# Performance work log

Hardware: AMD Instinct MI355X
Metric: run time of the kernel (lower is better)

The kernel has to match this reference:

```python
import jax, jax.numpy as jnp
import numpy as np

B, C, L = 16, 256, 2048

def setup_inputs() -> dict:
    key = jax.random.key(0)
    y = jax.random.normal(key, (B, C, L), dtype=jnp.float32)
    alpha = jnp.float32(0.5)
    beta = jnp.float32(0.5)
    gamma = jnp.float32(0.0)
    return {"y": y, "alpha": alpha, "beta": beta, "gamma": gamma}

def reference(y, alpha, beta, gamma):
    # y: [B, C, L]
    Bs, Cs, Ls = y.shape
    # channel attention: scores over channels, scaled by 1/sqrt(L)
    scale_c = 1.0 / np.sqrt(max(Ls, 1)).astype(np.float32)
    scores_c = jnp.einsum('bcl,bdl->bcd', y, y) * scale_c          # [B, C, C]
    attn_c = jax.nn.softmax(scores_c, axis=-1)
    y_c = jnp.einsum('bcd,bdl->bcl', attn_c, y)                    # [B, C, L]
    # time attention: scores over time steps, scaled by 1/sqrt(C)
    scale_t = 1.0 / np.sqrt(max(Cs, 1)).astype(np.float32)
    scores_t = jnp.einsum('bcl,bcm->blm', y, y) * scale_t          # [B, L, L]
    attn_t = jax.nn.softmax(scores_t, axis=-1)
    y_t = jnp.einsum('blm,bcm->bcl', attn_t, y)                    # [B, C, L]
    # learnable weighted combine + residual (gamma)
    out = alpha * y_c + beta * y_t + gamma * y
    return out
```

## Files before the change

kernel.cpp:

```cpp
#include <hip/hip_runtime.h>

#define B_ 16
#define C_ 256
#define L_ 2048

typedef __attribute__((ext_vector_type(8))) short short8;
typedef __attribute__((ext_vector_type(4))) float float4v;

__device__ inline float4v mfma16(short8 a, short8 b, float4v c) {
  return __builtin_amdgcn_mfma_f32_16x16x32_bf16(a, b, c, 0, 0, 0);
}

__device__ inline ushort f2bf(float x) {
  union { float f; unsigned u; } v; v.f = x;
  unsigned r = (v.u + 0x7fffu + ((v.u >> 16) & 1u)) >> 16;
  return (ushort)r;
}

__device__ inline float bf2f(ushort u) {
  union { unsigned u; float f; } v; v.u = ((unsigned)u) << 16;
  return v.f;
}

__device__ inline void dma16(const ushort* g, void* l) {
  __builtin_amdgcn_global_load_lds(
      (const __attribute__((address_space(1))) unsigned int*)(g),
      (__attribute__((address_space(3))) unsigned int*)(l), 16, 0, 0);
}

#define BAR_FULL() asm volatile("s_waitcnt vmcnt(0) lgkmcnt(0)\ns_barrier" ::: "memory")
#define BAR_LGKM() asm volatile("s_waitcnt lgkmcnt(0)\ns_barrier" ::: "memory")
#define BAR_VM8() asm volatile("s_waitcnt vmcnt(8)\ns_barrier" ::: "memory")
#define BAR_VM4() asm volatile("s_waitcnt vmcnt(4)\ns_barrier" ::: "memory")
#define BAR_VM0() asm volatile("s_waitcnt vmcnt(0)\ns_barrier" ::: "memory")
#define BAR_RAW() asm volatile("s_barrier" ::: "memory")

__global__ __launch_bounds__(256) void cvt_kernel(const float* __restrict__ y,
                                                  ushort* __restrict__ yb,
                                                  ushort* __restrict__ ytb) {
  __shared__ float tile[64][68];
  int b = blockIdx.z, ct = blockIdx.y, lt = blockIdx.x;
  int tx = threadIdx.x & 15, ty = threadIdx.x >> 4;
  size_t base = ((size_t)b * C_ + (size_t)ct * 64) * L_ + (size_t)lt * 64;
#pragma unroll
  for (int i = 0; i < 4; ++i) {
    int r = ty + i * 16;
    float4 v = *(const float4*)(y + base + (size_t)r * L_ + tx * 4);
    *(float4*)(&tile[r][tx * 4]) = v;
    ushort4 u;
    u.x = f2bf(v.x); u.y = f2bf(v.y); u.z = f2bf(v.z); u.w = f2bf(v.w);
    *(ushort4*)(yb + base + (size_t)r * L_ + tx * 4) = u;
  }
  __syncthreads();
  size_t tbase = ((size_t)b * L_ + (size_t)lt * 64) * C_ + (size_t)ct * 64;
#pragma unroll
  for (int i = 0; i < 4; ++i) {
    int r = ty + i * 16;
    ushort4 u;
    u.x = f2bf(tile[tx * 4 + 0][r]);
    u.y = f2bf(tile[tx * 4 + 1][r]);
    u.z = f2bf(tile[tx * 4 + 2][r]);
    u.w = f2bf(tile[tx * 4 + 3][r]);
    *(ushort4*)(ytb + tbase + (size_t)r * C_ + tx * 4) = u;
  }
}

__global__ __launch_bounds__(512) void pk_kernel(const ushort* __restrict__ yb,
                                                 ushort* __restrict__ Pc,
                                                 float* __restrict__ ginvC) {
  const int blk = blockIdx.x;
  const int b = (blk & 7) + 8 * ((blk >> 3) & 1);
  const int m0 = (blk >> 4) * 16;
  const int tid = threadIdx.x;
  const int w = tid >> 6, lane = tid & 63, quad = lane >> 4, l16 = lane & 15;
  const float scale = 0.022097086912079608f;
  const float SHIFT = 45.0f;

  __shared__ __align__(16) unsigned char Tb[3][32768];
  __shared__ float wsum[8][16];

  const ushort* Yb = yb + (size_t)b * C_ * L_;
  const int chq = ((lane & 3) - ((lane >> 3) & 3)) & 3;
  const int dl = (lane >> 2) * L_ + chq * 8;
  const int sK = (quad + ((l16 >> 1) & 3)) & 3;
  const int frag_lane = l16 * 64 + sK * 16;

  float4v acc[2];
#pragma unroll
  for (int nt = 0; nt < 2; ++nt) acc[nt] = (float4v){0.f, 0.f, 0.f, 0.f};

  auto PK_STAGE = [&](int t) {
    int kc = t * 64;
    unsigned char* bp = Tb[t % 3];
#pragma unroll
    for (int j = 0; j < 4; ++j) {
      int gi = w * 4 + j, kk2 = gi >> 4, chgrp = gi & 15;
      dma16(Yb + (size_t)chgrp * 16 * L_ + kc + kk2 * 32 + dl, (void*)(bp + gi * 1024));
    }
  };

  PK_STAGE(0);
  PK_STAGE(1);

  for (int c = 0; c < 32; ++c) {
    if (c == 31) { BAR_VM0(); } else { BAR_VM4(); }
    if (c < 30) PK_STAGE(c + 2);
    const unsigned char* cbuf = Tb[c % 3];
    __builtin_amdgcn_s_setprio(1);
#pragma unroll
    for (int kk2 = 0; kk2 < 2; ++kk2) {
      short8 aA = *(const short8*)(cbuf + (kk2 * 16 + (m0 >> 4)) * 1024 + frag_lane);
#pragma unroll
      for (int nt = 0; nt < 2; ++nt) {
        short8 bB = *(const short8*)(cbuf + (kk2 * 16 + w * 2 + nt) * 1024 + frag_lane);
        acc[nt] = mfma16(aA, bB, acc[nt]);
      }
    }
    __builtin_amdgcn_s_setprio(0);
  }

  float p[2][4], rs[4] = {0.f, 0.f, 0.f, 0.f};
#pragma unroll
  for (int nt = 0; nt < 2; ++nt)
#pragma unroll
    for (int r = 0; r < 4; ++r) {
      p[nt][r] = __expf(fmaf(acc[nt][r], scale, -SHIFT));
      rs[r] += p[nt][r];
    }
  ushort* Pb = Pc + ((size_t)b * 256 + m0) * 256;
#pragma unroll
  for (int nt = 0; nt < 2; ++nt)
#pragma unroll
    for (int r = 0; r < 4; ++r)
      Pb[(quad * 4 + r) * 256 + w * 32 + nt * 16 + l16] = f2bf(p[nt][r]);
#pragma unroll
  for (int r = 0; r < 4; ++r)
#pragma unroll
    for (int off = 1; off < 16; off <<= 1) rs[r] += __shfl_xor(rs[r], off);
  if (l16 == 0) {
#pragma unroll
    for (int r = 0; r < 4; ++r) wsum[w][quad * 4 + r] = rs[r];
  }
  __syncthreads();
  if (tid < 16) {
    float s = 0.f;
#pragma unroll
    for (int ww = 0; ww < 8; ++ww) s += wsum[ww][tid];
    ginvC[b * 256 + m0 + tid] = 1.0f / s;
  }
}

__global__ __launch_bounds__(256, 2) void ct_kernel(
    const ushort* __restrict__ yb, const ushort* __restrict__ ytb,
    const ushort* __restrict__ Pc, const float* __restrict__ ginvC,
    float* __restrict__ out, const float* __restrict__ alpha_p,
    const float* __restrict__ beta_p, const float* __restrict__ gamma_p) {
  const int blk = blockIdx.x;
  const int b = (blk & 7) + 8 * ((blk >> 3) & 1);
  const int m0 = (blk >> 4) * 64;
  const int tid = threadIdx.x;
  const int w = tid >> 6, lane = tid & 63, quad = lane >> 4, l16 = lane & 15;
  const int mtw = w >> 1, kt2 = w & 1;
  const float scale = 0.0625f;
  const float SHIFT = 16.0f;

  __shared__ __align__(16) unsigned char buf[2][32768];
  __shared__ ushort Pd[64 * 40];
  __shared__ float wsum[4][64];
  __shared__ float ginv[64];

  const ushort* Yt = ytb + (size_t)b * L_ * C_;
  const ushort* Yb = yb + (size_t)b * C_ * L_;
  const ushort* Pcb = Pc + (size_t)b * 256 * 256;
  const int chq = ((lane & 3) - ((lane >> 3) & 3)) & 3;
  const int klK = (lane >> 2) * C_ + chq * 8;
  const int vlV = (lane >> 2) * L_ + chq * 8;
  const int pcl = (lane >> 2) * 256 + chq * 8;
  const int sK = (quad + ((l16 >> 1) & 3)) & 3;
  const int frag_lane = l16 * 64 + sK * 16;

  short8 Qf[2][8];
#pragma unroll
  for (int mt = 0; mt < 2; ++mt)
#pragma unroll
    for (int kk = 0; kk < 8; ++kk)
      Qf[mt][kk] = *(const short8*)(Yt + (size_t)(m0 + mtw * 32 + mt * 16 + l16) * C_ +
                                    kk * 32 + quad * 8);
  const ushort* qgrow[2];
#pragma unroll
  for (int mt = 0; mt < 2; ++mt)
    qgrow[mt] = Yt + (size_t)(m0 + (1 - mtw) * 32 + mt * 16 + l16) * C_ + quad * 8;

  float4v fc[4][4];
#pragma unroll
  for (int mt = 0; mt < 4; ++mt)
#pragma unroll
    for (int nt = 0; nt < 4; ++nt) fc[mt][nt] = (float4v){0.f, 0.f, 0.f, 0.f};

  short8 qg[2][2];
#pragma unroll
  for (int mt = 0; mt < 2; ++mt) qg[0][mt] = *(const short8*)(qgrow[mt]);
#pragma unroll
  for (int j = 0; j < 4; ++j) {
    int gi = w * 4 + j;
    dma16(Pcb + (size_t)(gi * 16) * 256 + pcl, (void*)(buf[0] + gi * 1024));
  }

  for (int c2 = 0; c2 < 8; ++c2) {
    const int cb = c2 & 1;
    BAR_FULL();
    if (c2 < 7) {
      unsigned char* bp = buf[cb ^ 1];
#pragma unroll
      for (int j = 0; j < 4; ++j) {
        int gi = w * 4 + j;
        dma16(Pcb + (size_t)(gi * 16) * 256 + (c2 + 1) * 32 + pcl,
              (void*)(bp + gi * 1024));
      }
#pragma unroll
      for (int mt = 0; mt < 2; ++mt)
        qg[cb ^ 1][mt] = *(const short8*)(qgrow[mt] + (c2 + 1) * 32);
    }
    __builtin_amdgcn_s_setprio(1);
#pragma unroll
    for (int mt = 0; mt < 4; ++mt) {
      short8 Ac = *(const short8*)(buf[cb] + (w * 4 + mt) * 1024 + frag_lane);
#pragma unroll
      for (int nt = 0; nt < 4; ++nt) {
        short8 Bq = ((nt >> 1) == mtw) ? Qf[nt & 1][c2] : qg[cb][nt & 1];
        fc[mt][nt] = mfma16(Ac, Bq, fc[mt][nt]);
      }
    }
    __builtin_amdgcn_s_setprio(0);
  }

  const ushort* dp[8];
#pragma unroll
  for (int j = 0; j < 8; ++j) {
    int gi = w * 8 + j;
    if (gi < 16) {
      int kk = gi >> 1, g = gi & 1;
      dp[j] = Yt + (size_t)(g * 16) * C_ + kk * 32 + klK;
    } else {
      int cg = gi - 16;
      dp[j] = Yb + (size_t)cg * 16 * L_ + vlV;
    }
  }
  const int dstride = (w < 2) ? 32 * C_ : 32;

  float4v ft[4][4];
#pragma unroll
  for (int mt = 0; mt < 4; ++mt)
#pragma unroll
    for (int nt = 0; nt < 4; ++nt) ft[mt][nt] = (float4v){0.f, 0.f, 0.f, 0.f};
  float rs[2][4] = {{0.f, 0.f, 0.f, 0.f}, {0.f, 0.f, 0.f, 0.f}};

#pragma unroll
  for (int j = 0; j < 8; ++j) {
    dma16(dp[j], (void*)(buf[0] + (w * 8 + j) * 1024));
    dp[j] += dstride;
  }
  BAR_RAW();
#pragma unroll
  for (int j = 0; j < 8; ++j) {
    dma16(dp[j], (void*)(buf[1] + (w * 8 + j) * 1024));
    dp[j] += dstride;
  }

  for (int c = 0; c < 64; ++c) {
    const int cb = c & 1;
    if (c == 63) { BAR_VM0(); } else { BAR_VM8(); }
    float4v s0 = (float4v){0.f, 0.f, 0.f, 0.f};
    float4v s1 = (float4v){0.f, 0.f, 0.f, 0.f};
    __builtin_amdgcn_s_setprio(1);
#pragma unroll
    for (int kk = 0; kk < 8; ++kk) {
      short8 bf = *(const short8*)(buf[cb] + (kk * 2 + kt2) * 1024 + frag_lane);
      s0 = mfma16(Qf[0][kk], bf, s0);
      s1 = mfma16(Qf[1][kk], bf, s1);
    }
    __builtin_amdgcn_s_setprio(0);
#pragma unroll
    for (int mt = 0; mt < 2; ++mt) {
      float4v s = mt ? s1 : s0;
#pragma unroll
      for (int r = 0; r < 4; ++r) {
        float p = __expf(fmaf(s[r], scale, -SHIFT));
        rs[mt][r] += p;
        Pd[(mtw * 32 + mt * 16 + quad * 4 + r) * 40 + kt2 * 16 + l16] = f2bf(p);
      }
    }
    BAR_LGKM();
    __builtin_amdgcn_s_setprio(1);
#pragma unroll
    for (int mt = 0; mt < 4; ++mt) {
      short8 va = *(const short8*)(buf[cb] + (16 + w * 4 + mt) * 1024 + frag_lane);
#pragma unroll
      for (int nt = 0; nt < 4; ++nt) {
        short8 pb = *(const short8*)(&Pd[(nt * 16 + l16) * 40 + quad * 8]);
        ft[mt][nt] = mfma16(va, pb, ft[mt][nt]);
      }
    }
    __builtin_amdgcn_s_setprio(0);
    BAR_RAW();
    if (c < 62) {
#pragma unroll
      for (int j = 0; j < 8; ++j) {
        dma16(dp[j], (void*)(buf[cb] + (w * 8 + j) * 1024));
        dp[j] += dstride;
      }
    }
  }

  __syncthreads();
#pragma unroll
  for (int mt = 0; mt < 2; ++mt)
#pragma unroll
    for (int r = 0; r < 4; ++r)
#pragma unroll
      for (int off = 1; off < 16; off <<= 1) rs[mt][r] += __shfl_xor(rs[mt][r], off);
  if (l16 == 0) {
#pragma unroll
    for (int mt = 0; mt < 2; ++mt)
#pragma unroll
      for (int r = 0; r < 4; ++r)
        wsum[w][mtw * 32 + mt * 16 + quad * 4 + r] = rs[mt][r];
  }
  __syncthreads();
  if (tid < 64) {
    int mh = tid >> 5;
    ginv[tid] = 1.0f / (wsum[mh * 2][tid] + wsum[mh * 2 + 1][tid]);
  }
  __syncthreads();

  const float alpha = alpha_p[0], beta = beta_p[0], gamma = gamma_p[0];
  float gq[4];
#pragma unroll
  for (int nt = 0; nt < 4; ++nt) gq[nt] = beta * ginv[nt * 16 + l16];
  float gc[4][4];
#pragma unroll
  for (int mt = 0; mt < 4; ++mt)
#pragma unroll
    for (int r = 0; r < 4; ++r)
      gc[mt][r] = alpha * ginvC[b * 256 + w * 64 + mt * 16 + quad * 4 + r];

  if (gamma != 0.0f) {
#pragma unroll
    for (int mt = 0; mt < 4; ++mt)
#pragma unroll
      for (int nt = 0; nt < 4; ++nt)
#pragma unroll
        for (int r = 0; r < 4; ++r) {
          int ch = w * 64 + mt * 16 + quad * 4 + r;
          size_t idx = ((size_t)b * C_ + ch) * L_ + m0 + nt * 16 + l16;
          float v = gc[mt][r] * fc[mt][nt][r] + gq[nt] * ft[mt][nt][r];
          out[idx] = fmaf(gamma, bf2f(Yb[(size_t)ch * L_ + m0 + nt * 16 + l16]), v);
        }
  } else {
#pragma unroll
    for (int mt = 0; mt < 4; ++mt)
#pragma unroll
      for (int nt = 0; nt < 4; ++nt)
#pragma unroll
        for (int r = 0; r < 4; ++r) {
          int ch = w * 64 + mt * 16 + quad * 4 + r;
          size_t idx = ((size_t)b * C_ + ch) * L_ + m0 + nt * 16 + l16;
          out[idx] = gc[mt][r] * fc[mt][nt][r] + gq[nt] * ft[mt][nt][r];
        }
  }
}

extern "C" void kernel_launch(void* const* d_in, const int* in_sizes, int n_in,
                              void* d_out, int out_size, void* d_ws, size_t ws_size,
                              hipStream_t stream) {
  const float* y = (const float*)d_in[0];
  const float* alpha = (const float*)d_in[1];
  const float* beta = (const float*)d_in[2];
  const float* gamma = (const float*)d_in[3];
  float* out = (float*)d_out;

  ushort* yb = (ushort*)d_ws;
  ushort* ytb = yb + (size_t)B_ * C_ * L_;
  ushort* Pc = ytb + (size_t)B_ * C_ * L_;
  float* ginvC = (float*)(Pc + (size_t)B_ * 256 * 256);

  hipLaunchKernelGGL(cvt_kernel, dim3(L_ / 64, C_ / 64, B_), dim3(256), 0, stream,
                     y, yb, ytb);
  hipLaunchKernelGGL(pk_kernel, dim3(256), dim3(512), 0, stream, yb, Pc, ginvC);
  hipLaunchKernelGGL(ct_kernel, dim3(512), dim3(256), 0, stream,
                     yb, ytb, Pc, ginvC, out, alpha, beta, gamma);
}
```

Measured before the change: 205.1 us.

## Give each wave its own 16 query columns, passing P through registers

Restructures ct_kernel so each wave owns 16 query time steps across all 256 channels instead of a 2x2 split of queries and key halves. The softmax probabilities now go straight from the score MFMA output registers into the PV MFMA operand, with no LDS staging buffer. This removes the per-iteration LDS write/read and one barrier, and shrinks the row-sum reduction to a single LDS pass. It also reworks the Pc prefetch into a two-deep DMA pipeline and permutes K row loading to match the register layout. In exchange each wave loads all 16 K tiles and all 16 V tiles per step, so LDS read traffic per wave grows. It also relies on a register-layout trick and on lgkm-only waits in place of barriers, which must be correct.

```diff
diff --git a/kernel.cpp b/kernel.cpp
--- a/kernel.cpp
+++ b/kernel.cpp
@@ -29,11 +29,12 @@
 }
 
 #define BAR_FULL() asm volatile("s_waitcnt vmcnt(0) lgkmcnt(0)\ns_barrier" ::: "memory")
-#define BAR_LGKM() asm volatile("s_waitcnt lgkmcnt(0)\ns_barrier" ::: "memory")
 #define BAR_VM8() asm volatile("s_waitcnt vmcnt(8)\ns_barrier" ::: "memory")
 #define BAR_VM4() asm volatile("s_waitcnt vmcnt(4)\ns_barrier" ::: "memory")
 #define BAR_VM0() asm volatile("s_waitcnt vmcnt(0)\ns_barrier" ::: "memory")
 #define BAR_RAW() asm volatile("s_barrier" ::: "memory")
+#define WAIT_VM0() asm volatile("s_waitcnt vmcnt(0)" ::: "memory")
+#define WAIT_LGKM0() asm volatile("s_waitcnt lgkmcnt(0)" ::: "memory")
 
 __global__ __launch_bounds__(256) void cvt_kernel(const float* __restrict__ y,
                                                   ushort* __restrict__ yb,
@@ -160,79 +161,26 @@
   const int m0 = (blk >> 4) * 64;
   const int tid = threadIdx.x;
   const int w = tid >> 6, lane = tid & 63, quad = lane >> 4, l16 = lane & 15;
-  const int mtw = w >> 1, kt2 = w & 1;
-  const float scale = 0.0625f;
+  const float scale_t = 0.0625f;
   const float SHIFT = 16.0f;
 
   __shared__ __align__(16) unsigned char buf[2][32768];
-  __shared__ ushort Pd[64 * 40];
-  __shared__ float wsum[4][64];
-  __shared__ float ginv[64];
+  __shared__ float rsum[256];
 
   const ushort* Yt = ytb + (size_t)b * L_ * C_;
   const ushort* Yb = yb + (size_t)b * C_ * L_;
   const ushort* Pcb = Pc + (size_t)b * 256 * 256;
   const int chq = ((lane & 3) - ((lane >> 3) & 3)) & 3;
-  const int klK = (lane >> 2) * C_ + chq * 8;
   const int vlV = (lane >> 2) * L_ + chq * 8;
   const int pcl = (lane >> 2) * 256 + chq * 8;
   const int sK = (quad + ((l16 >> 1) & 3)) & 3;
   const int frag_lane = l16 * 64 + sK * 16;
-
-  short8 Qf[2][8];
-#pragma unroll
-  for (int mt = 0; mt < 2; ++mt)
-#pragma unroll
-    for (int kk = 0; kk < 8; ++kk)
-      Qf[mt][kk] = *(const short8*)(Yt + (size_t)(m0 + mtw * 32 + mt * 16 + l16) * C_ +
-                                    kk * 32 + quad * 8);
-  const ushort* qgrow[2];
-#pragma unroll
-  for (int mt = 0; mt < 2; ++mt)
-    qgrow[mt] = Yt + (size_t)(m0 + (1 - mtw) * 32 + mt * 16 + l16) * C_ + quad * 8;
-
-  float4v fc[4][4];
-#pragma unroll
-  for (int mt = 0; mt < 4; ++mt)
-#pragma unroll
-    for (int nt = 0; nt < 4; ++nt) fc[mt][nt] = (float4v){0.f, 0.f, 0.f, 0.f};
-
-  short8 qg[2][2];
-#pragma unroll
-  for (int mt = 0; mt < 2; ++mt) qg[0][mt] = *(const short8*)(qgrow[mt]);
-#pragma unroll
-  for (int j = 0; j < 4; ++j) {
-    int gi = w * 4 + j;
-    dma16(Pcb + (size_t)(gi * 16) * 256 + pcl, (void*)(buf[0] + gi * 1024));
-  }
-
-  for (int c2 = 0; c2 < 8; ++c2) {
-    const int cb = c2 & 1;
-    BAR_FULL();
-    if (c2 < 7) {
-      unsigned char* bp = buf[cb ^ 1];
-#pragma unroll
-      for (int j = 0; j < 4; ++j) {
-        int gi = w * 4 + j;
-        dma16(Pcb + (size_t)(gi * 16) * 256 + (c2 + 1) * 32 + pcl,
-              (void*)(bp + gi * 1024));
-      }
-#pragma unroll
-      for (int mt = 0; mt < 2; ++mt)
-        qg[cb ^ 1][mt] = *(const short8*)(qgrow[mt] + (c2 + 1) * 32);
-    }
-    __builtin_amdgcn_s_setprio(1);
-#pragma unroll
-    for (int mt = 0; mt < 4; ++mt) {
-      short8 Ac = *(const short8*)(buf[cb] + (w * 4 + mt) * 1024 + frag_lane);
-#pragma unroll
-      for (int nt = 0; nt < 4; ++nt) {
-        short8 Bq = ((nt >> 1) == mtw) ? Qf[nt & 1][c2] : qg[cb][nt & 1];
-        fc[mt][nt] = mfma16(Ac, Bq, fc[mt][nt]);
-      }
-    }
-    __builtin_amdgcn_s_setprio(0);
-  }
+  const int qcol = m0 + w * 16 + l16;
+
+  short8 Qf[8];
+#pragma unroll
+  for (int kk = 0; kk < 8; ++kk)
+    Qf[kk] = *(const short8*)(Yt + (size_t)qcol * C_ + kk * 32 + quad * 8);
 
   const ushort* dp[8];
 #pragma unroll
@@ -240,7 +188,9 @@
     int gi = w * 8 + j;
     if (gi < 16) {
       int kk = gi >> 1, g = gi & 1;
-      dp[j] = Yt + (size_t)(g * 16) * C_ + kk * 32 + klK;
+      int ridx = lane >> 2;
+      int trow = g * 4 + (ridx & 3) + (ridx >> 2) * 8;
+      dp[j] = Yt + (size_t)trow * C_ + kk * 32 + chq * 8;
     } else {
       int cg = gi - 16;
       dp[j] = Yb + (size_t)cg * 16 * L_ + vlV;
@@ -248,24 +198,60 @@
   }
   const int dstride = (w < 2) ? 32 * C_ : 32;
 
-  float4v ft[4][4];
-#pragma unroll
-  for (int mt = 0; mt < 4; ++mt)
-#pragma unroll
-    for (int nt = 0; nt < 4; ++nt) ft[mt][nt] = (float4v){0.f, 0.f, 0.f, 0.f};
-  float rs[2][4] = {{0.f, 0.f, 0.f, 0.f}, {0.f, 0.f, 0.f, 0.f}};
-
-#pragma unroll
-  for (int j = 0; j < 8; ++j) {
-    dma16(dp[j], (void*)(buf[0] + (w * 8 + j) * 1024));
-    dp[j] += dstride;
-  }
-  BAR_RAW();
+  WAIT_VM0();
+
+  float4v fc[16];
+#pragma unroll
+  for (int ct = 0; ct < 16; ++ct) fc[ct] = (float4v){0.f, 0.f, 0.f, 0.f};
+
+#pragma unroll
+  for (int j = 0; j < 4; ++j) {
+    int gi = w * 4 + j;
+    dma16(Pcb + (size_t)(gi * 16) * 256 + pcl, (void*)(buf[0] + gi * 1024));
+  }
+#pragma unroll
+  for (int j = 0; j < 4; ++j) {
+    int gi = w * 4 + j;
+    dma16(Pcb + (size_t)(gi * 16) * 256 + 32 + pcl, (void*)(buf[1] + gi * 1024));
+  }
+
+  for (int c2 = 0; c2 < 8; ++c2) {
+    const int cb = c2 & 1;
+    if (c2 == 7) { BAR_VM0(); } else { BAR_VM4(); }
+    if (c2 == 7) {
+#pragma unroll
+      for (int j = 0; j < 8; ++j) {
+        dma16(dp[j], (void*)(buf[0] + (w * 8 + j) * 1024));
+        dp[j] += dstride;
+      }
+    }
+    __builtin_amdgcn_s_setprio(1);
+#pragma unroll
+    for (int ct = 0; ct < 16; ++ct) {
+      short8 Ac = *(const short8*)(buf[cb] + ct * 1024 + frag_lane);
+      fc[ct] = mfma16(Ac, Qf[c2], fc[ct]);
+    }
+    __builtin_amdgcn_s_setprio(0);
+    BAR_RAW();
+    if (c2 < 6) {
+#pragma unroll
+      for (int j = 0; j < 4; ++j) {
+        int gi = w * 4 + j;
+        dma16(Pcb + (size_t)(gi * 16) * 256 + (c2 + 2) * 32 + pcl,
+              (void*)(buf[cb] + gi * 1024));
+      }
+    }
+  }
 #pragma unroll
   for (int j = 0; j < 8; ++j) {
     dma16(dp[j], (void*)(buf[1] + (w * 8 + j) * 1024));
     dp[j] += dstride;
   }
+
+  float4v ft[16];
+#pragma unroll
+  for (int ct = 0; ct < 16; ++ct) ft[ct] = (float4v){0.f, 0.f, 0.f, 0.f};
+  float rs = 0.f;
 
   for (int c = 0; c < 64; ++c) {
     const int cb = c & 1;
@@ -275,31 +261,28 @@
     __builtin_amdgcn_s_setprio(1);
 #pragma unroll
     for (int kk = 0; kk < 8; ++kk) {
-      short8 bf = *(const short8*)(buf[cb] + (kk * 2 + kt2) * 1024 + frag_lane);
-      s0 = mfma16(Qf[0][kk], bf, s0);
-      s1 = mfma16(Qf[1][kk], bf, s1);
+      short8 k0 = *(const short8*)(buf[cb] + (kk * 2 + 0) * 1024 + frag_lane);
+      short8 k1 = *(const short8*)(buf[cb] + (kk * 2 + 1) * 1024 + frag_lane);
+      s0 = mfma16(k0, Qf[kk], s0);
+      s1 = mfma16(k1, Qf[kk], s1);
     }
     __builtin_amdgcn_s_setprio(0);
-#pragma unroll
-    for (int mt = 0; mt < 2; ++mt) {
-      float4v s = mt ? s1 : s0;
-#pragma unroll
-      for (int r = 0; r < 4; ++r) {
-        float p = __expf(fmaf(s[r], scale, -SHIFT));
-        rs[mt][r] += p;
-        Pd[(mtw * 32 + mt * 16 + quad * 4 + r) * 40 + kt2 * 16 + l16] = f2bf(p);
-      }
-    }
-    BAR_LGKM();
+    union PU { ushort us[8]; short8 v; } pu;
+    float p0, p1;
+#pragma unroll
+    for (int r = 0; r < 4; ++r) {
+      p0 = __expf(fmaf(s0[r], scale_t, -SHIFT));
+      p1 = __expf(fmaf(s1[r], scale_t, -SHIFT));
+      rs += p0 + p1;
+      pu.us[r] = f2bf(p0);
+      pu.us[4 + r] = f2bf(p1);
+    }
+    short8 pb = pu.v;
     __builtin_amdgcn_s_setprio(1);
 #pragma unroll
-    for (int mt = 0; mt < 4; ++mt) {
-      short8 va = *(const short8*)(buf[cb] + (16 + w * 4 + mt) * 1024 + frag_lane);
-#pragma unroll
-      for (int nt = 0; nt < 4; ++nt) {
-        short8 pb = *(const short8*)(&Pd[(nt * 16 + l16) * 40 + quad * 8]);
-        ft[mt][nt] = mfma16(va, pb, ft[mt][nt]);
-      }
+    for (int ct = 0; ct < 16; ++ct) {
+      short8 va = *(const short8*)(buf[cb] + (16 + ct) * 1024 + frag_lane);
+      ft[ct] = mfma16(va, pb, ft[ct]);
     }
     __builtin_amdgcn_s_setprio(0);
     BAR_RAW();
@@ -312,61 +295,39 @@
     }
   }
 
-  __syncthreads();
-#pragma unroll
-  for (int mt = 0; mt < 2; ++mt)
-#pragma unroll
-    for (int r = 0; r < 4; ++r)
-#pragma unroll
-      for (int off = 1; off < 16; off <<= 1) rs[mt][r] += __shfl_xor(rs[mt][r], off);
-  if (l16 == 0) {
-#pragma unroll
-    for (int mt = 0; mt < 2; ++mt)
-#pragma unroll
-      for (int r = 0; r < 4; ++r)
-        wsum[w][mtw * 32 + mt * 16 + quad * 4 + r] = rs[mt][r];
-  }
-  __syncthreads();
-  if (tid < 64) {
-    int mh = tid >> 5;
-    ginv[tid] = 1.0f / (wsum[mh * 2][tid] + wsum[mh * 2 + 1][tid]);
-  }
-  __syncthreads();
+  rsum[tid] = rs;
+  WAIT_LGKM0();
+  float rstot = rsum[w * 64 + l16] + rsum[w * 64 + 16 + l16] +
+                rsum[w * 64 + 32 + l16] + rsum[w * 64 + 48 + l16];
 
   const float alpha = alpha_p[0], beta = beta_p[0], gamma = gamma_p[0];
-  float gq[4];
-#pragma unroll
-  for (int nt = 0; nt < 4; ++nt) gq[nt] = beta * ginv[nt * 16 + l16];
-  float gc[4][4];
-#pragma unroll
-  for (int mt = 0; mt < 4; ++mt)
-#pragma unroll
-    for (int r = 0; r < 4; ++r)
-      gc[mt][r] = alpha * ginvC[b * 256 + w * 64 + mt * 16 + quad * 4 + r];
+  const float gq = beta / rstot;
 
   if (gamma != 0.0f) {
 #pragma unroll
-    for (int mt = 0; mt < 4; ++mt)
-#pragma unroll
-      for (int nt = 0; nt < 4; ++nt)
-#pragma unroll
-        for (int r = 0; r < 4; ++r) {
-          int ch = w * 64 + mt * 16 + quad * 4 + r;
-          size_t idx = ((size_t)b * C_ + ch) * L_ + m0 + nt * 16 + l16;
-          float v = gc[mt][r] * fc[mt][nt][r] + gq[nt] * ft[mt][nt][r];
-          out[idx] = fmaf(gamma, bf2f(Yb[(size_t)ch * L_ + m0 + nt * 16 + l16]), v);
-        }
+    for (int ct = 0; ct < 16; ++ct) {
+      float4 gcv = *(const float4*)(ginvC + b * 256 + ct * 16 + quad * 4);
+#pragma unroll
+      for (int r = 0; r < 4; ++r) {
+        int ch = ct * 16 + quad * 4 + r;
+        size_t idx = ((size_t)b * C_ + ch) * L_ + qcol;
+        float g = (r == 0) ? gcv.x : (r == 1) ? gcv.y : (r == 2) ? gcv.z : gcv.w;
+        float v = alpha * g * fc[ct][r] + gq * ft[ct][r];
+        out[idx] = fmaf(gamma, bf2f(Yb[(size_t)ch * L_ + qcol]), v);
+      }
+    }
   } else {
 #pragma unroll
-    for (int mt = 0; mt < 4; ++mt)
-#pragma unroll
-      for (int nt = 0; nt < 4; ++nt)
-#pragma unroll
-        for (int r = 0; r < 4; ++r) {
-          int ch = w * 64 + mt * 16 + quad * 4 + r;
-          size_t idx = ((size_t)b * C_ + ch) * L_ + m0 + nt * 16 + l16;
-          out[idx] = gc[mt][r] * fc[mt][nt][r] + gq[nt] * ft[mt][nt][r];
-        }
+    for (int ct = 0; ct < 16; ++ct) {
+      float4 gcv = *(const float4*)(ginvC + b * 256 + ct * 16 + quad * 4);
+#pragma unroll
+      for (int r = 0; r < 4; ++r) {
+        int ch = ct * 16 + quad * 4 + r;
+        size_t idx = ((size_t)b * C_ + ch) * L_ + qcol;
+        float g = (r == 0) ? gcv.x : (r == 1) ? gcv.y : (r == 2) ? gcv.z : gcv.w;
+        out[idx] = alpha * g * fc[ct][r] + gq * ft[ct][r];
+      }
+    }
   }
 }
 
```

Measured after the change: 201.7 us. No clear change (-1.7%).
